# Kernel optimization log

Measured on AMD Instinct MI355X. Metric: run time of the kernel, lower is better.

## Reference

```python
import jax, jax.numpy as jnp
import numpy as np
import math

DIM = 512
HEADS = 8
DH = DIM // HEADS          # 64 = dim_head
M = 17                     # num_landmarks
PINV_ITERS = 6
RES_K = 33                 # residual depthwise conv kernel (lucidrains default)


def layer_norm(x, g, b, eps=1e-5):
    mu = x.mean(-1, keepdims=True)
    var = ((x - mu) ** 2).mean(-1, keepdims=True)
    return (x - mu) * jax.lax.rsqrt(var + eps) * g + b


def dwconv2d(x, w, b, k):
    # x: [B,C,H,W], w: [C,1,k,k] depthwise
    p = k // 2
    y = jax.lax.conv_general_dilated(x, w, (1, 1), ((p, p), (p, p)),
        dimension_numbers=('NCHW', 'OIHW', 'NCHW'), feature_group_count=x.shape[1])
    return y + b[None, :, None, None]


def moore_penrose_pinv(x, iters=PINV_ITERS):
    ax = jnp.abs(x)
    z = jnp.swapaxes(x, -1, -2) / (jnp.max(ax.sum(-1)) * jnp.max(ax.sum(-2)))
    I = jnp.eye(x.shape[-1], dtype=x.dtype)
    for _ in range(iters):
        xz = x @ z
        z = 0.25 * z @ (13 * I - xz @ (15 * I - xz @ (7 * I - xz)))
    return z


def nystrom_attn(x, qkv_w, out_w, out_b, res_w):
    # lucidrains NystromAttention, eval mode (dropout=identity), return_attn=True
    b, n, _ = x.shape
    pad = (M - n % M) % M
    xp = jnp.pad(x, ((0, 0), (pad, 0), (0, 0)))  # pad at FRONT
    q, k, v = jnp.split(xp @ qkv_w, 3, axis=-1)
    to_heads = lambda t: t.reshape(b, -1, HEADS, DH).transpose(0, 2, 1, 3)  # b h n d
    q, k, v = to_heads(q), to_heads(k), to_heads(v)
    q = q * (DH ** -0.5)
    l = (n + pad) // M
    ql = q.reshape(b, HEADS, M, l, DH).mean(3)  # landmarks b h m d
    kl = k.reshape(b, HEADS, M, l, DH).mean(3)
    a1 = jax.nn.softmax(jnp.einsum('bhid,bhjd->bhij', q, kl), axis=-1)   # [b,h,n,m]
    a2 = jax.nn.softmax(jnp.einsum('bhid,bhjd->bhij', ql, kl), axis=-1)  # [b,h,m,m]
    a3 = jax.nn.softmax(jnp.einsum('bhid,bhjd->bhij', ql, k), axis=-1)   # [b,h,m,n]
    a2i = moore_penrose_pinv(a2)
    left = a1 @ a2i                       # [b,h,n,m]
    out = left @ (a3 @ v)                 # [b,h,n,d]
    # residual depthwise conv over heads, kernel (33,1) along seq
    res = jax.lax.conv_general_dilated(v, res_w, (1, 1), ((RES_K // 2, RES_K // 2), (0, 0)),
        dimension_numbers=('NCHW', 'OIHW', 'NCHW'), feature_group_count=HEADS)
    out = out + res
    out = out.transpose(0, 2, 1, 3).reshape(b, -1, DIM)
    out = out @ out_w + out_b
    attn = left @ a3                      # [b,h,n_pad,n_pad]
    return out[:, -n:], attn


def ppeg(x, H, W, w7, b7, w5, b5, w3, b3):
    B, _, C = x.shape
    cls_t, feat = x[:, :1], x[:, 1:]
    cnn = feat.transpose(0, 2, 1).reshape(B, C, H, W)
    y = dwconv2d(cnn, w7, b7, 7) + cnn + dwconv2d(cnn, w5, b5, 5) + dwconv2d(cnn, w3, b3, 3)
    y = y.reshape(B, C, H * W).transpose(0, 2, 1)
    return jnp.concatenate([cls_t, y], axis=1)


def setup_inputs():
    key = jax.random.key(0)
    ks = jax.random.split(key, 20)
    B, N, IN, NC = 2, 2048, 1024, 2
    s = 0.02
    d = {}
    d['feats'] = jax.random.normal(ks[0], (B, N, IN), jnp.float32)
    d['fc1_w'] = jax.random.normal(ks[1], (IN, DIM), jnp.float32) * s
    d['fc1_b'] = jnp.zeros((DIM,), jnp.float32)
    d['cls_token'] = jax.random.normal(ks[2], (1, 1, DIM), jnp.float32)
    for i, pre in enumerate(['l1', 'l2']):
        o = 3 + i * 3
        d[pre + '_norm_g'] = jnp.ones((DIM,), jnp.float32)
        d[pre + '_norm_b'] = jnp.zeros((DIM,), jnp.float32)
        d[pre + '_qkv_w'] = jax.random.normal(ks[o], (DIM, 3 * DIM), jnp.float32) * s
        d[pre + '_out_w'] = jax.random.normal(ks[o + 1], (DIM, DIM), jnp.float32) * s
        d[pre + '_out_b'] = jnp.zeros((DIM,), jnp.float32)
        d[pre + '_res_w'] = jax.random.normal(ks[o + 2], (HEADS, 1, RES_K, 1), jnp.float32) * s
    for kk, kidx in zip([7, 5, 3], [9, 10, 11]):
        d['ppeg_w%d' % kk] = jax.random.normal(ks[kidx], (DIM, 1, kk, kk), jnp.float32) * s
        d['ppeg_b%d' % kk] = jnp.zeros((DIM,), jnp.float32)
    d['norm_g'] = jnp.ones((DIM,), jnp.float32)
    d['norm_b'] = jnp.zeros((DIM,), jnp.float32)
    d['fc2_w'] = jax.random.normal(ks[12], (DIM, NC), jnp.float32) * s
    d['fc2_b'] = jnp.zeros((NC,), jnp.float32)
    return d


def reference(feats, fc1_w, fc1_b, cls_token,
              l1_norm_g, l1_norm_b, l1_qkv_w, l1_out_w, l1_out_b, l1_res_w,
              l2_norm_g, l2_norm_b, l2_qkv_w, l2_out_w, l2_out_b, l2_res_w,
              ppeg_w7, ppeg_b7, ppeg_w5, ppeg_b5, ppeg_w3, ppeg_b3,
              norm_g, norm_b, fc2_w, fc2_b):
    h = jax.nn.relu(feats @ fc1_w + fc1_b)          # [B,N,512]
    N = h.shape[1]
    Hs = int(math.ceil(math.sqrt(N)))               # square grid side
    add = Hs * Hs - N
    h = jnp.concatenate([h, h[:, :add]], axis=1)    # duplicate-pad to Hs*Hs
    B = h.shape[0]
    h = jnp.concatenate([jnp.broadcast_to(cls_token, (B, 1, DIM)), h], axis=1)
    a1, aw1 = nystrom_attn(layer_norm(h, l1_norm_g, l1_norm_b), l1_qkv_w, l1_out_w, l1_out_b, l1_res_w)
    h = h + a1
    h = ppeg(h, Hs, Hs, ppeg_w7, ppeg_b7, ppeg_w5, ppeg_b5, ppeg_w3, ppeg_b3)
    a2, aw2 = nystrom_attn(layer_norm(h, l2_norm_g, l2_norm_b), l2_qkv_w, l2_out_w, l2_out_b, l2_res_w)
    h = h + a2
    h = layer_norm(h, norm_g, norm_b)[:, 0]
    logits = h @ fc2_w + fc2_b
    return logits, aw1, aw2
```

## Files before the change

### kernel.cpp

```cpp
#include <hip/hip_runtime.h>
#include <math.h>
#include <stdint.h>

#define BATCH 2
#define NIN   1024
#define NSEQ  2048
#define DIMC  512
#define NH    8
#define DHD   64
#define MLM   17
#define LBLK  125
#define SEQ   2117
#define NPAD  2125
#define PAD0  8
#define HS    46
#define NPIX  2116
#define RA    4250
#define AWSZ  ((size_t)BATCH*NH*NPAD*NPAD)

typedef _Float16 half8 __attribute__((ext_vector_type(8)));
typedef float    floatx4 __attribute__((ext_vector_type(4)));

__device__ __forceinline__ void store_hl(_Float16* __restrict__ xh, _Float16* __restrict__ xl,
                                         int c, int ra, float v)
{
    _Float16 hv = (_Float16)v;
    size_t o = ((size_t)(c >> 3) * RA + ra) * 8 + (c & 7);
    xh[o] = hv;
    xl[o] = (_Float16)(v - (float)hv);
}

__global__ void convA_kernel(const float* __restrict__ X, _Float16* __restrict__ hi,
                             _Float16* __restrict__ lo, int R, int K)
{
    int GK = K >> 3;
    size_t idx = (size_t)blockIdx.x * 256 + threadIdx.x;
    if (idx >= (size_t)R * GK) return;
    int r = (int)(idx % R); int gk = (int)(idx / R);
    const float* s = X + (size_t)r * K + gk * 8;
    half8 h, l;
    #pragma unroll
    for (int j = 0; j < 8; ++j) {
        float x = s[j];
        _Float16 hh = (_Float16)x;
        h[j] = hh;
        l[j] = (_Float16)(x - (float)hh);
    }
    *(half8*)(hi + idx * 8) = h;
    *(half8*)(lo + idx * 8) = l;
}

__global__ void convB_kernel(const float* __restrict__ X, _Float16* __restrict__ hi,
                             _Float16* __restrict__ lo, int N, int K)
{
    int GK = K >> 3;
    size_t idx = (size_t)blockIdx.x * 256 + threadIdx.x;
    if (idx >= (size_t)N * GK) return;
    int n = (int)(idx % N); int gk = (int)(idx / N);
    const float* s = X + (size_t)(gk * 8) * N + n;
    half8 h, l;
    #pragma unroll
    for (int j = 0; j < 8; ++j) {
        float x = s[(size_t)j * N];
        _Float16 hh = (_Float16)x;
        h[j] = hh;
        l[j] = (_Float16)(x - (float)hh);
    }
    *(half8*)(hi + idx * 8) = h;
    *(half8*)(lo + idx * 8) = l;
}

__global__ __launch_bounds__(256) void gemm_mfma(
    const _Float16* __restrict__ Ah, const _Float16* __restrict__ Al,
    const _Float16* __restrict__ Bh, const _Float16* __restrict__ Bl,
    const float* __restrict__ bias, float* __restrict__ C,
    int Mn, int Nn, int Kn, int relu,
    int split, float* __restrict__ qp, float* __restrict__ kp, float* __restrict__ vp)
{
    __shared__ _Float16 sA[2][2][4][128][8];
    __shared__ _Float16 sB[2][2][4][128][8];
    const int tid = threadIdx.x;
    const int wv = tid >> 6, ln = tid & 63;
    const int m0 = blockIdx.y * 128, n0 = blockIdx.x * 128;
    const int wm = (wv >> 1) * 64, wn = (wv & 1) * 64;
    const int g = ln >> 4, rr = ln & 15;

    floatx4 acc[4][4];
    #pragma unroll
    for (int m = 0; m < 4; ++m)
        #pragma unroll
        for (int n = 0; n < 4; ++n)
            acc[m][n] = (floatx4){0.f, 0.f, 0.f, 0.f};

    auto STAGE = [&](int bf, int gk0) {
        #pragma unroll
        for (int q2 = 0; q2 < 8; ++q2) {
            int c = wv + q2 * 4;
            int arr = c >> 3, gg = (c >> 1) & 3, hf = c & 1;
            const _Float16* base = (arr == 0) ? Ah : (arr == 1) ? Al : (arr == 2) ? Bh : Bl;
            int Rdim = (arr < 2) ? Mn : Nn;
            int rg = ((arr < 2) ? m0 : n0) + hf * 64 + ln;
            if (arr < 2 && rg >= Mn) rg = Mn - 1;
            const _Float16* src = base + ((size_t)(gk0 + gg) * Rdim + rg) * 8;
            _Float16* dst = (arr == 0) ? &sA[bf][0][gg][hf * 64][0] :
                            (arr == 1) ? &sA[bf][1][gg][hf * 64][0] :
                            (arr == 2) ? &sB[bf][0][gg][hf * 64][0] :
                                         &sB[bf][1][gg][hf * 64][0];
            __builtin_amdgcn_global_load_lds(
                (__attribute__((address_space(1))) void*)(uintptr_t)src,
                (__attribute__((address_space(3))) void*)dst, 16, 0, 0);
        }
    };

    const int nt = Kn >> 5;
    STAGE(0, 0);
    __syncthreads();
    for (int t = 0; t < nt; ++t) {
        const int cur = t & 1;
        if (t + 1 < nt) STAGE(cur ^ 1, (t + 1) * 4);
        half8 a_h[4], a_l[4], b_h[4], b_l[4];
        #pragma unroll
        for (int m = 0; m < 4; ++m) {
            a_h[m] = *(const half8*)&sA[cur][0][g][wm + m * 16 + rr][0];
            a_l[m] = *(const half8*)&sA[cur][1][g][wm + m * 16 + rr][0];
        }
        #pragma unroll
        for (int n = 0; n < 4; ++n) {
            b_h[n] = *(const half8*)&sB[cur][0][g][wn + n * 16 + rr][0];
            b_l[n] = *(const half8*)&sB[cur][1][g][wn + n * 16 + rr][0];
        }
        #pragma unroll
        for (int m = 0; m < 4; ++m)
            #pragma unroll
            for (int n = 0; n < 4; ++n) {
                acc[m][n] = __builtin_amdgcn_mfma_f32_16x16x32_f16(a_h[m], b_h[n], acc[m][n], 0, 0, 0);
                acc[m][n] = __builtin_amdgcn_mfma_f32_16x16x32_f16(a_l[m], b_h[n], acc[m][n], 0, 0, 0);
                acc[m][n] = __builtin_amdgcn_mfma_f32_16x16x32_f16(a_h[m], b_l[n], acc[m][n], 0, 0, 0);
            }
        __syncthreads();
    }

    const int rq = ln >> 4;
    if (!split) {
        #pragma unroll
        for (int n = 0; n < 4; ++n) {
            int col = n0 + wn + n * 16 + rr;
            float bv = bias ? bias[col] : 0.f;
            #pragma unroll
            for (int m = 0; m < 4; ++m) {
                #pragma unroll
                for (int r = 0; r < 4; ++r) {
                    int row = m0 + wm + m * 16 + rq * 4 + r;
                    if (row < Mn) {
                        float vv = acc[m][n][r] + bv;
                        if (relu) vv = fmaxf(vv, 0.f);
                        C[(size_t)row * Nn + col] = vv;
                    }
                }
            }
        }
    } else {
        #pragma unroll
        for (int n = 0; n < 4; ++n) {
            int col = n0 + wn + n * 16 + rr;
            int sect = col >> 9, hh = (col >> 6) & 7, dd = col & 63;
            float* dstb = (sect == 0) ? qp : (sect == 1) ? kp : vp;
            float sc = (sect == 0) ? 0.125f : 1.f;
            #pragma unroll
            for (int m = 0; m < 4; ++m) {
                #pragma unroll
                for (int r = 0; r < 4; ++r) {
                    int row = m0 + wm + m * 16 + rq * 4 + r;
                    if (row < Mn) {
                        int b = (row >= NPAD) ? 1 : 0;
                        int i = row - b * NPAD;
                        dstb[(((size_t)(b * NH + hh)) * NPAD + i) * DHD + dd] = acc[m][n][r] * sc;
                    }
                }
            }
        }
    }
}

__global__ void buildh_kernel(const float* __restrict__ h0, const float* __restrict__ cls,
                              float* __restrict__ h)
{
    size_t e4 = (size_t)blockIdx.x*256 + threadIdx.x;
    if (e4 >= (size_t)BATCH*SEQ*DIMC/4) return;
    int c4 = (int)(e4 % (DIMC/4)); size_t r = e4 / (DIMC/4);
    int t = (int)(r % SEQ); int b = (int)(r / SEQ);
    float4 val;
    if (t == 0) val = ((const float4*)cls)[c4];
    else {
        int n = t - 1;
        if (n >= NSEQ) n -= NSEQ;
        val = ((const float4*)h0)[((size_t)(b*NSEQ + n))*(DIMC/4) + c4];
    }
    ((float4*)h)[e4] = val;
}

__global__ void ln_pad_kernel(const float* __restrict__ h, const float* __restrict__ g,
                              const float* __restrict__ bta,
                              _Float16* __restrict__ xh, _Float16* __restrict__ xl)
{
    int r = blockIdx.x; int b = blockIdx.y; int t = threadIdx.x;
    int ra = b*NPAD + r;
    if (r < PAD0) {
        store_hl(xh, xl, t, ra, 0.f);
        store_hl(xh, xl, t + 256, ra, 0.f);
        return;
    }
    const float* x = &h[((size_t)(b*SEQ + r-PAD0))*DIMC];
    __shared__ float ws[4];
    int wid = t >> 6, ln = t & 63;
    float x0 = x[t], x1 = x[t+256];
    float s = x0 + x1;
    #pragma unroll
    for (int m = 1; m < 64; m <<= 1) s += __shfl_xor(s, m, 64);
    if (ln == 0) ws[wid] = s;
    __syncthreads();
    float mu = (ws[0]+ws[1]+ws[2]+ws[3]) * (1.f/512.f);
    float d0 = x0-mu, d1 = x1-mu;
    float vv = d0*d0 + d1*d1;
    #pragma unroll
    for (int m = 1; m < 64; m <<= 1) vv += __shfl_xor(vv, m, 64);
    __syncthreads();
    if (ln == 0) ws[wid] = vv;
    __syncthreads();
    float rstd = 1.0f / sqrtf((ws[0]+ws[1]+ws[2]+ws[3])*(1.f/512.f) + 1e-5f);
    store_hl(xh, xl, t,       ra, d0*rstd*g[t]     + bta[t]);
    store_hl(xh, xl, t + 256, ra, d1*rstd*g[t+256] + bta[t+256]);
}

__global__ void landmark_kernel(const float* __restrict__ q, const float* __restrict__ k,
                                float* __restrict__ ql, float* __restrict__ kl)
{
    int m = blockIdx.x, h = blockIdx.y, b = blockIdx.z, d = threadIdx.x;
    int bh = b*NH + h;
    size_t base = ((size_t)bh*NPAD + m*LBLK)*DHD + d;
    float sq = 0.f, sk = 0.f;
    for (int r=0;r<LBLK;++r){ sq += q[base + (size_t)r*DHD]; sk += k[base + (size_t)r*DHD]; }
    size_t o = ((size_t)bh*MLM + m)*DHD + d;
    ql[o] = sq / 125.f; kl[o] = sk / 125.f;
}

__global__ void a1_left_kernel(const float* __restrict__ q, const float* __restrict__ kl,
                               const float* __restrict__ a2i, float* __restrict__ left)
{
    int i = blockIdx.x, h = blockIdx.y, b = blockIdx.z;
    int bh = b*NH + h; int lane = threadIdx.x;
    __shared__ alignas(16) float qrow[64];
    __shared__ float dots[MLM];
    __shared__ float arow[MLM];
    qrow[lane] = q[((size_t)bh*NPAD + i)*DHD + lane];
    __syncthreads();
    if (lane < MLM) {
        const float4* kr4 = (const float4*)&kl[((size_t)bh*MLM + lane)*DHD];
        const float4* q4 = (const float4*)qrow;
        float acc = 0.f;
        #pragma unroll
        for (int d4=0; d4<16; ++d4) {
            float4 a = q4[d4], bb = kr4[d4];
            acc += a.x*bb.x + a.y*bb.y + a.z*bb.z + a.w*bb.w;
        }
        dots[lane] = acc;
    }
    __syncthreads();
    if (lane < MLM) {
        float mx = -1e30f;
        for (int u=0;u<MLM;++u) mx = fmaxf(mx, dots[u]);
        float s = 0.f;
        for (int u=0;u<MLM;++u) s += expf(dots[u]-mx);
        arow[lane] = expf(dots[lane]-mx)/s;
    }
    __syncthreads();
    if (lane < MLM) {
        const float* zi = &a2i[(size_t)bh*MLM*MLM];
        float acc = 0.f;
        for (int k2=0;k2<MLM;++k2) acc += arow[k2]*zi[k2*MLM + lane];
        left[((size_t)bh*NPAD + i)*MLM + lane] = acc;
    }
}

__global__ void a2_kernel(const float* __restrict__ ql, const float* __restrict__ kl,
                          float* __restrict__ a2)
{
    int bh = blockIdx.x; int t = threadIdx.x;
    __shared__ float s[MLM*MLM];
    if (t < MLM*MLM) {
        int m = t/MLM, j = t%MLM;
        const float* qr = &ql[((size_t)bh*MLM+m)*DHD];
        const float* kr = &kl[((size_t)bh*MLM+j)*DHD];
        float acc=0.f; for(int d=0;d<DHD;++d) acc += qr[d]*kr[d];
        s[t] = acc;
    }
    __syncthreads();
    if (t < MLM*MLM) {
        int m = t/MLM;
        float mx=-1e30f; for(int u=0;u<MLM;++u) mx=fmaxf(mx, s[m*MLM+u]);
        float sm=0.f; for(int u=0;u<MLM;++u) sm += expf(s[m*MLM+u]-mx);
        a2[(size_t)bh*MLM*MLM + t] = expf(s[t]-mx)/sm;
    }
}

__global__ void a3_kernel(const float* __restrict__ ql, const float* __restrict__ k,
                          float* __restrict__ a3)
{
    int m = blockIdx.x, h = blockIdx.y, b = blockIdx.z;
    int bh = b*NH + h; int tid = threadIdx.x;
    __shared__ alignas(16) float qlrow[64];
    __shared__ float buf[NPAD];
    __shared__ float red[256];
    if (tid < 64) qlrow[tid] = ql[((size_t)bh*MLM+m)*DHD + tid];
    __syncthreads();
    for (int j = tid; j < NPAD; j += 256) {
        const float4* kr4 = (const float4*)&k[((size_t)bh*NPAD + j)*DHD];
        const float4* q4 = (const float4*)qlrow;
        float acc = 0.f;
        #pragma unroll
        for (int d4=0; d4<16; ++d4) {
            float4 kk = kr4[d4], qq = q4[d4];
            acc += qq.x*kk.x + qq.y*kk.y + qq.z*kk.z + qq.w*kk.w;
        }
        buf[j] = acc;
    }
    __syncthreads();
    float mx = -1e30f;
    for (int j = tid; j < NPAD; j += 256) mx = fmaxf(mx, buf[j]);
    red[tid] = mx; __syncthreads();
    for (int s=128;s>0;s>>=1){ if(tid<s) red[tid]=fmaxf(red[tid],red[tid+s]); __syncthreads(); }
    mx = red[0]; __syncthreads();
    float sm = 0.f;
    for (int j = tid; j < NPAD; j += 256) sm += expf(buf[j]-mx);
    red[tid] = sm; __syncthreads();
    for (int s=128;s>0;s>>=1){ if(tid<s) red[tid]+=red[tid+s]; __syncthreads(); }
    sm = red[0];
    for (int j = tid; j < NPAD; j += 256)
        a3[((size_t)bh*MLM+m)*NPAD + j] = expf(buf[j]-mx)/sm;
}

__global__ void pinv_kernel(const float* __restrict__ a2, float* __restrict__ a2i)
{
    int bh = blockIdx.x; int t = threadIdx.x;
    __shared__ float x[289], z[289], xz[289], w1[289], w2[289];
    __shared__ float red[320], red2[320];
    float rs = -1e30f, cs = -1e30f;
    if (t < BATCH*NH*MLM) {
        int m2 = t/MLM, i2 = t%MLM;
        const float* xx = &a2[(size_t)m2*MLM*MLM];
        float r=0.f, c=0.f;
        for (int j=0;j<MLM;++j){ r += fabsf(xx[i2*MLM+j]); c += fabsf(xx[j*MLM+i2]); }
        rs = r; cs = c;
    }
    red[t] = rs; red2[t] = cs; __syncthreads();
    for (int s=256;s>0;s>>=1){
        if (t<s && t+s<320){ red[t]=fmaxf(red[t],red[t+s]); red2[t]=fmaxf(red2[t],red2[t+s]); }
        __syncthreads();
    }
    float scal = 1.f/(red[0]*red2[0]);

    int i = t/MLM, j = t%MLM;
    bool act = t < MLM*MLM;
    if (act) x[t] = a2[(size_t)bh*MLM*MLM + t];
    __syncthreads();
    if (act) z[t] = x[j*MLM+i] * scal;
    __syncthreads();
    for (int it=0; it<6; ++it) {
        if (act){ float a=0.f; for(int k2=0;k2<MLM;++k2) a += x[i*MLM+k2]*z[k2*MLM+j]; xz[t]=a; }
        __syncthreads();
        if (act){ w1[t] = (i==j?7.f:0.f) - xz[t]; }
        __syncthreads();
        if (act){ float a=0.f; for(int k2=0;k2<MLM;++k2) a += xz[i*MLM+k2]*w1[k2*MLM+j]; w2[t]=a; }
        __syncthreads();
        if (act){ w1[t] = (i==j?15.f:0.f) - w2[t]; }
        __syncthreads();
        if (act){ float a=0.f; for(int k2=0;k2<MLM;++k2) a += xz[i*MLM+k2]*w1[k2*MLM+j]; w2[t]=a; }
        __syncthreads();
        if (act){ w1[t] = (i==j?13.f:0.f) - w2[t]; }
        __syncthreads();
        if (act){ float a=0.f; for(int k2=0;k2<MLM;++k2) a += z[i*MLM+k2]*w1[k2*MLM+j]; w2[t]=0.25f*a; }
        __syncthreads();
        if (act) z[t] = w2[t];
        __syncthreads();
    }
    if (act) a2i[(size_t)bh*MLM*MLM + t] = z[t];
}

__global__ void a3v_kernel(const float* __restrict__ a3, const float* __restrict__ v,
                           float* __restrict__ a3v)
{
    int m = blockIdx.x, h = blockIdx.y, b = blockIdx.z, d = threadIdx.x;
    int bh = b*NH + h;
    const float* ar = &a3[((size_t)bh*MLM+m)*NPAD];
    const float* vb = &v[(size_t)bh*NPAD*DHD + d];
    float acc = 0.f;
    for (int j=0;j<NPAD;++j) acc += ar[j]*vb[(size_t)j*DHD];
    a3v[((size_t)bh*MLM+m)*DHD + d] = acc;
}

__global__ void headout_kernel(const float* __restrict__ left, const float* __restrict__ a3v,
                               const float* __restrict__ v, const float* __restrict__ res_w,
                               _Float16* __restrict__ hh, _Float16* __restrict__ hl)
{
    int i = blockIdx.x, h = blockIdx.y, b = blockIdx.z, t = threadIdx.x;
    int bh = b*NH + h;
    __shared__ float lrow[MLM];
    __shared__ float rw[33];
    if (t < MLM) lrow[t] = left[((size_t)bh*NPAD+i)*MLM+t];
    if (t < 33)  rw[t] = res_w[h*33 + t];
    __syncthreads();
    float acc = 0.f;
    for (int m2=0;m2<MLM;++m2) acc += lrow[m2]*a3v[((size_t)bh*MLM+m2)*DHD+t];
    for (int s=0;s<33;++s) {
        int ii = i + s - 16;
        if (ii >= 0 && ii < NPAD) acc += rw[s]*v[((size_t)bh*NPAD+ii)*DHD+t];
    }
    store_hl(hh, hl, h*DHD + t, b*NPAD + i, acc);
}

__global__ __launch_bounds__(256) void attn_out_kernel(const float* __restrict__ left,
                                                       const float* __restrict__ a3,
                                                       float* __restrict__ aw)
{
    int bh = blockIdx.z; int i0 = blockIdx.y*64; int j0 = blockIdx.x*512;
    int t = threadIdx.x;
    __shared__ float lrows[64][20];
    for (int u = t; u < 64*MLM; u += 256) {
        int ii = u / MLM, kk = u % MLM;
        int gi = i0 + ii;
        lrows[ii][kk] = (gi < NPAD) ? left[((size_t)bh*NPAD + gi)*MLM + kk] : 0.f;
    }
    __syncthreads();
    int j1 = j0 + t, j2 = j0 + 256 + t;
    float c1[MLM], c2[MLM];
    #pragma unroll
    for (int kk = 0; kk < MLM; ++kk) {
        c1[kk] = (j1 < NPAD) ? a3[((size_t)bh*MLM + kk)*NPAD + j1] : 0.f;
        c2[kk] = (j2 < NPAD) ? a3[((size_t)bh*MLM + kk)*NPAD + j2] : 0.f;
    }
    int imax = NPAD - i0; if (imax > 64) imax = 64;
    for (int ii = 0; ii < imax; ++ii) {
        float lv[17];
        *(float4*)&lv[0]  = *(const float4*)&lrows[ii][0];
        *(float4*)&lv[4]  = *(const float4*)&lrows[ii][4];
        *(float4*)&lv[8]  = *(const float4*)&lrows[ii][8];
        *(float4*)&lv[12] = *(const float4*)&lrows[ii][12];
        lv[16] = lrows[ii][16];
        float s1 = 0.f, s2 = 0.f;
        #pragma unroll
        for (int kk = 0; kk < MLM; ++kk) { s1 += lv[kk]*c1[kk]; s2 += lv[kk]*c2[kk]; }
        size_t ob = ((size_t)bh*NPAD + (i0+ii))*NPAD;
        if (j1 < NPAD) aw[ob + j1] = s1;
        if (j2 < NPAD) aw[ob + j2] = s2;
    }
}

__global__ void add_res_kernel(float* __restrict__ h, const float* __restrict__ proj)
{
    size_t e4 = (size_t)blockIdx.x*256 + threadIdx.x;
    if (e4 >= (size_t)BATCH*SEQ*DIMC/4) return;
    int c4 = (int)(e4 % (DIMC/4)); size_t r = e4 / (DIMC/4);
    int tt = (int)(r % SEQ); int b = (int)(r / SEQ);
    float4 p = ((const float4*)proj)[((size_t)(b*NPAD + PAD0 + tt))*(DIMC/4) + c4];
    float4* hp = &((float4*)h)[e4];
    float4 hv = *hp;
    hv.x += p.x; hv.y += p.y; hv.z += p.z; hv.w += p.w;
    *hp = hv;
}

__global__ void transpose_h2im(const float* __restrict__ h, float* __restrict__ im)
{
    __shared__ float tile[32][33];
    int p0 = blockIdx.x*32, c0 = blockIdx.y*32, b = blockIdx.z;
    int tx = threadIdx.x & 31, ty = threadIdx.x >> 5;
    #pragma unroll
    for (int i=0;i<32;i+=8) {
        int p = p0 + ty + i;
        if (p < NPIX) tile[ty+i][tx] = h[((size_t)(b*SEQ) + 1 + p)*DIMC + c0 + tx];
    }
    __syncthreads();
    #pragma unroll
    for (int i=0;i<32;i+=8) {
        int c = c0 + ty + i, p = p0 + tx;
        if (p < NPIX) im[((size_t)(b*DIMC) + c)*NPIX + p] = tile[tx][ty+i];
    }
}

__global__ void ppeg_conv_kernel(const float* __restrict__ im,
                                 const float* __restrict__ w7, const float* __restrict__ b7,
                                 const float* __restrict__ w5, const float* __restrict__ b5,
                                 const float* __restrict__ w3, const float* __restrict__ b3,
                                 float* __restrict__ im2)
{
    int c = blockIdx.x; int b = blockIdx.y; int t = threadIdx.x;
    __shared__ float img[NPIX];
    __shared__ float wf[49+25+9];
    const float* src = &im[((size_t)(b*DIMC+c))*NPIX];
    for (int p=t; p<NPIX; p+=256) img[p] = src[p];
    if (t < 49) wf[t] = w7[c*49+t];
    else if (t >= 64 && t < 64+25) wf[49 + (t-64)] = w5[c*25 + (t-64)];
    else if (t >= 96 && t < 96+9)  wf[74 + (t-96)] = w3[c*9 + (t-96)];
    __syncthreads();
    float bias = b7[c] + b5[c] + b3[c];
    for (int p=t; p<NPIX; p+=256) {
        int y = p/HS, x = p%HS;
        float acc = img[p] + bias;
        for (int dy=-3; dy<=3; ++dy){ int yy=y+dy; if (yy<0||yy>=HS) continue;
            for (int dx=-3; dx<=3; ++dx){ int xx=x+dx; if (xx<0||xx>=HS) continue;
                acc += wf[(dy+3)*7+(dx+3)]*img[yy*HS+xx]; } }
        for (int dy=-2; dy<=2; ++dy){ int yy=y+dy; if (yy<0||yy>=HS) continue;
            for (int dx=-2; dx<=2; ++dx){ int xx=x+dx; if (xx<0||xx>=HS) continue;
                acc += wf[49+(dy+2)*5+(dx+2)]*img[yy*HS+xx]; } }
        for (int dy=-1; dy<=1; ++dy){ int yy=y+dy; if (yy<0||yy>=HS) continue;
            for (int dx=-1; dx<=1; ++dx){ int xx=x+dx; if (xx<0||xx>=HS) continue;
                acc += wf[74+(dy+1)*3+(dx+1)]*img[yy*HS+xx]; } }
        im2[((size_t)(b*DIMC)+c)*NPIX + p] = acc;
    }
}

__global__ void transpose_im2h(const float* __restrict__ im2, float* __restrict__ h)
{
    __shared__ float tile[32][33];
    int p0 = blockIdx.x*32, c0 = blockIdx.y*32, b = blockIdx.z;
    int tx = threadIdx.x & 31, ty = threadIdx.x >> 5;
    #pragma unroll
    for (int i=0;i<32;i+=8) {
        int c = c0 + ty + i, p = p0 + tx;
        if (p < NPIX) tile[ty+i][tx] = im2[((size_t)(b*DIMC) + c)*NPIX + p];
    }
    __syncthreads();
    #pragma unroll
    for (int i=0;i<32;i+=8) {
        int p = p0 + ty + i;
        if (p < NPIX) h[((size_t)(b*SEQ) + 1 + p)*DIMC + c0 + tx] = tile[tx][ty+i];
    }
}

__global__ void final_kernel(const float* __restrict__ h, const float* __restrict__ g,
                             const float* __restrict__ bta, const float* __restrict__ fc2w,
                             const float* __restrict__ fc2b, float* __restrict__ out)
{
    int b = blockIdx.x; int t = threadIdx.x;
    __shared__ float red[512];
    const float* x = &h[(size_t)b*SEQ*DIMC];
    float xv = x[t];
    red[t] = xv; __syncthreads();
    for (int s=256;s>0;s>>=1){ if(t<s) red[t]+=red[t+s]; __syncthreads(); }
    float mu = red[0]/512.f; __syncthreads();
    float d = xv - mu;
    red[t] = d*d; __syncthreads();
    for (int s=256;s>0;s>>=1){ if(t<s) red[t]+=red[t+s]; __syncthreads(); }
    float var = red[0]/512.f; __syncthreads();
    float hn = d * (1.f/sqrtf(var+1e-5f)) * g[t] + bta[t];
    for (int c=0;c<2;++c) {
        red[t] = hn * fc2w[t*2+c]; __syncthreads();
        for (int s=256;s>0;s>>=1){ if(t<s) red[t]+=red[t+s]; __syncthreads(); }
        if (t==0) out[b*2+c] = red[0] + fc2b[c];
        __syncthreads();
    }
}

extern "C" void kernel_launch(void* const* d_in, const int* in_sizes, int n_in,
                              void* d_out, int out_size, void* d_ws, size_t ws_size,
                              hipStream_t stream)
{
    (void)in_sizes; (void)n_in; (void)out_size; (void)ws_size;
    const float* feats = (const float*)d_in[0];
    const float* fc1_w = (const float*)d_in[1];
    const float* fc1_b = (const float*)d_in[2];
    const float* cls   = (const float*)d_in[3];
    const float* ln_g[2]  = {(const float*)d_in[4],  (const float*)d_in[10]};
    const float* ln_b[2]  = {(const float*)d_in[5],  (const float*)d_in[11]};
    const float* qkv_w[2] = {(const float*)d_in[6],  (const float*)d_in[12]};
    const float* out_w[2] = {(const float*)d_in[7],  (const float*)d_in[13]};
    const float* out_b[2] = {(const float*)d_in[8],  (const float*)d_in[14]};
    const float* res_w[2] = {(const float*)d_in[9],  (const float*)d_in[15]};
    const float* w7 = (const float*)d_in[16]; const float* b7 = (const float*)d_in[17];
    const float* w5 = (const float*)d_in[18]; const float* b5 = (const float*)d_in[19];
    const float* w3 = (const float*)d_in[20]; const float* b3 = (const float*)d_in[21];
    const float* ng = (const float*)d_in[22]; const float* nb = (const float*)d_in[23];
    const float* fc2w = (const float*)d_in[24]; const float* fc2b = (const float*)d_in[25];

    float* ws = (float*)d_ws;
    size_t off = 0;
    float* h    = ws + off; off += (size_t)BATCH*SEQ*DIMC;
    float* h0   = ws + off; off += (size_t)BATCH*NSEQ*DIMC;
    float* scr  = ws + off; off += (size_t)BATCH*NPAD*1536;
    float* q    = ws + off; off += (size_t)BATCH*NH*NPAD*DHD;
    float* k    = ws + off; off += (size_t)BATCH*NH*NPAD*DHD;
    float* v    = ws + off; off += (size_t)BATCH*NH*NPAD*DHD;
    float* ql   = ws + off; off += (size_t)BATCH*NH*MLM*DHD;
    float* kl   = ws + off; off += (size_t)BATCH*NH*MLM*DHD;
    float* a2   = ws + off; off += (size_t)BATCH*NH*MLM*MLM + 15;
    float* a2i  = ws + off; off += (size_t)BATCH*NH*MLM*MLM + 15;
    float* a3   = ws + off; off += (size_t)BATCH*NH*MLM*NPAD;
    float* left = ws + off; off += (size_t)BATCH*NH*NPAD*MLM;
    float* a3v  = ws + off; off += (size_t)BATCH*NH*MLM*DHD;
    _Float16* XAh = (_Float16*)(ws + off); off += 2097152;
    _Float16* XAl = (_Float16*)(ws + off); off += 2097152;
    _Float16* WBh = (_Float16*)(ws + off); off += 393216;
    _Float16* WBl = (_Float16*)(ws + off); off += 393216;
    float* proj = scr;
    float* im   = scr + (size_t)BATCH*NPAD*DIMC;
    float* im2  = im  + (size_t)BATCH*DIMC*NPIX;

    float* outp = (float*)d_out;

    convA_kernel<<<((size_t)4096*128+255)/256, 256, 0, stream>>>(feats, XAh, XAl, 4096, NIN);
    convB_kernel<<<((size_t)512*128+255)/256, 256, 0, stream>>>(fc1_w, WBh, WBl, DIMC, NIN);
    gemm_mfma<<<dim3(DIMC/128, 4096/128), 256, 0, stream>>>(
        XAh, XAl, WBh, WBl, fc1_b, h0, BATCH*NSEQ, DIMC, NIN, 1, 0, nullptr, nullptr, nullptr);
    {
        size_t tot4 = (size_t)BATCH*SEQ*DIMC/4;
        buildh_kernel<<<(tot4+255)/256, 256, 0, stream>>>(h0, cls, h);
    }

    for (int L = 0; L < 2; ++L) {
        float* aw = outp + 4 + (size_t)L*AWSZ;
        ln_pad_kernel<<<dim3(NPAD, BATCH), 256, 0, stream>>>(h, ln_g[L], ln_b[L], XAh, XAl);
        convB_kernel<<<((size_t)1536*64+255)/256, 256, 0, stream>>>(qkv_w[L], WBh, WBl, 1536, DIMC);
        gemm_mfma<<<dim3(1536/128, (RA+127)/128), 256, 0, stream>>>(
            XAh, XAl, WBh, WBl, nullptr, nullptr, RA, 1536, DIMC, 0, 1, q, k, v);
        landmark_kernel<<<dim3(MLM, NH, BATCH), 64, 0, stream>>>(q, k, ql, kl);
        a2_kernel<<<dim3(BATCH*NH), 320, 0, stream>>>(ql, kl, a2);
        a3_kernel<<<dim3(MLM, NH, BATCH), 256, 0, stream>>>(ql, k, a3);
        pinv_kernel<<<BATCH*NH, 320, 0, stream>>>(a2, a2i);
        a1_left_kernel<<<dim3(NPAD, NH, BATCH), 64, 0, stream>>>(q, kl, a2i, left);
        a3v_kernel<<<dim3(MLM, NH, BATCH), 64, 0, stream>>>(a3, v, a3v);
        headout_kernel<<<dim3(NPAD, NH, BATCH), 64, 0, stream>>>(left, a3v, v, res_w[L], XAh, XAl);
        attn_out_kernel<<<dim3((NPAD+511)/512, (NPAD+63)/64, BATCH*NH), 256, 0, stream>>>(left, a3, aw);
        convB_kernel<<<((size_t)512*64+255)/256, 256, 0, stream>>>(out_w[L], WBh, WBl, DIMC, DIMC);
        gemm_mfma<<<dim3(DIMC/128, (RA+127)/128), 256, 0, stream>>>(
            XAh, XAl, WBh, WBl, out_b[L], proj, RA, DIMC, DIMC, 0, 0, nullptr, nullptr, nullptr);
        {
            size_t tot4 = (size_t)BATCH*SEQ*DIMC/4;
            add_res_kernel<<<(tot4+255)/256, 256, 0, stream>>>(h, proj);
        }
        if (L == 0) {
            transpose_h2im<<<dim3((NPIX+31)/32, DIMC/32, BATCH), 256, 0, stream>>>(h, im);
            ppeg_conv_kernel<<<dim3(DIMC, BATCH), 256, 0, stream>>>(im, w7, b7, w5, b5, w3, b3, im2);
            transpose_im2h<<<dim3((NPIX+31)/32, DIMC/32, BATCH), 256, 0, stream>>>(im2, h);
        }
    }
    final_kernel<<<BATCH, 512, 0, stream>>>(h, ng, nb, fc2w, fc2b, outp);
}
```

Before: 1.364 ms.

## Fuse attention small kernels, GEMM epilogues, and batch weight conversions

Converts all five weight matrices to hi/lo fp16 in one launch. The fc1 GEMM epilogue now writes straight into the padded sequence buffer (cls row plus wrap duplicates), and the out-projection GEMM epilogue adds into the residual in place, which removes the buildh and add_res kernels. a2 is folded into pinv, a3v into a3, and a1_left into headout, and landmark uses 4 waves. This cuts launches and intermediate memory traffic. In exchange some blocks do redundant work: every pinv block recomputes all 16 a2 matrices.

```diff
diff --git a/kernel.cpp b/kernel.cpp
--- a/kernel.cpp
+++ b/kernel.cpp
@@ -16,7 +16,15 @@
 #define HS    46
 #define NPIX  2116
 #define RA    4250
+#define WRAP  68
 #define AWSZ  ((size_t)BATCH*NH*NPAD*NPAD)
+
+#define WOFF_FC1  0
+#define WOFF_QKV0 524288
+#define WOFF_QKV1 1310720
+#define WOFF_OUT0 2097152
+#define WOFF_OUT1 2359296
+#define WTOT      2621440
 
 typedef _Float16 half8 __attribute__((ext_vector_type(8)));
 typedef float    floatx4 __attribute__((ext_vector_type(4)));
@@ -31,51 +39,65 @@
 }
 
 __global__ void convA_kernel(const float* __restrict__ X, _Float16* __restrict__ hi,
-                             _Float16* __restrict__ lo, int R, int K)
-{
-    int GK = K >> 3;
+                             _Float16* __restrict__ lo, const float* __restrict__ cls,
+                             float* __restrict__ h)
+{
+    const int R = 4096, K = NIN, GK = K >> 3;
+    if (blockIdx.x == 0) {
+        int b = threadIdx.x >> 7, c4 = threadIdx.x & 127;
+        ((float4*)h)[((size_t)(b * SEQ)) * (DIMC/4) + c4] = ((const float4*)cls)[c4];
+    }
     size_t idx = (size_t)blockIdx.x * 256 + threadIdx.x;
     if (idx >= (size_t)R * GK) return;
     int r = (int)(idx % R); int gk = (int)(idx / R);
     const float* s = X + (size_t)r * K + gk * 8;
-    half8 h, l;
+    half8 hv, lv;
     #pragma unroll
     for (int j = 0; j < 8; ++j) {
         float x = s[j];
         _Float16 hh = (_Float16)x;
-        h[j] = hh;
-        l[j] = (_Float16)(x - (float)hh);
-    }
-    *(half8*)(hi + idx * 8) = h;
-    *(half8*)(lo + idx * 8) = l;
-}
-
-__global__ void convB_kernel(const float* __restrict__ X, _Float16* __restrict__ hi,
-                             _Float16* __restrict__ lo, int N, int K)
-{
+        hv[j] = hh;
+        lv[j] = (_Float16)(x - (float)hh);
+    }
+    *(half8*)(hi + idx * 8) = hv;
+    *(half8*)(lo + idx * 8) = lv;
+}
+
+__global__ void convW_kernel(const float* __restrict__ s0, const float* __restrict__ s1,
+                             const float* __restrict__ s2, const float* __restrict__ s3,
+                             const float* __restrict__ s4,
+                             _Float16* __restrict__ Wh, _Float16* __restrict__ Wl)
+{
+    int job = blockIdx.y;
+    const float* S; int N, K; size_t doff;
+    if      (job == 0) { S = s0; N = 512;  K = 1024; doff = WOFF_FC1;  }
+    else if (job == 1) { S = s1; N = 1536; K = 512;  doff = WOFF_QKV0; }
+    else if (job == 2) { S = s2; N = 1536; K = 512;  doff = WOFF_QKV1; }
+    else if (job == 3) { S = s3; N = 512;  K = 512;  doff = WOFF_OUT0; }
+    else               { S = s4; N = 512;  K = 512;  doff = WOFF_OUT1; }
     int GK = K >> 3;
     size_t idx = (size_t)blockIdx.x * 256 + threadIdx.x;
     if (idx >= (size_t)N * GK) return;
     int n = (int)(idx % N); int gk = (int)(idx / N);
-    const float* s = X + (size_t)(gk * 8) * N + n;
-    half8 h, l;
+    const float* s = S + (size_t)(gk * 8) * N + n;
+    half8 hv, lv;
     #pragma unroll
     for (int j = 0; j < 8; ++j) {
         float x = s[(size_t)j * N];
         _Float16 hh = (_Float16)x;
-        h[j] = hh;
-        l[j] = (_Float16)(x - (float)hh);
-    }
-    *(half8*)(hi + idx * 8) = h;
-    *(half8*)(lo + idx * 8) = l;
+        hv[j] = hh;
+        lv[j] = (_Float16)(x - (float)hh);
+    }
+    *(half8*)(Wh + doff + idx * 8) = hv;
+    *(half8*)(Wl + doff + idx * 8) = lv;
 }
 
 __global__ __launch_bounds__(256) void gemm_mfma(
     const _Float16* __restrict__ Ah, const _Float16* __restrict__ Al,
     const _Float16* __restrict__ Bh, const _Float16* __restrict__ Bl,
     const float* __restrict__ bias, float* __restrict__ C,
-    int Mn, int Nn, int Kn, int relu,
-    int split, float* __restrict__ qp, float* __restrict__ kp, float* __restrict__ vp)
+    int Mn, int Nn, int Kn, int mode,
+    float* __restrict__ qp, float* __restrict__ kp, float* __restrict__ vp)
 {
     __shared__ _Float16 sA[2][2][4][128][8];
     __shared__ _Float16 sB[2][2][4][128][8];
@@ -141,20 +163,41 @@
     }
 
     const int rq = ln >> 4;
-    if (!split) {
+    if (mode == 2) {
         #pragma unroll
         for (int n = 0; n < 4; ++n) {
             int col = n0 + wn + n * 16 + rr;
-            float bv = bias ? bias[col] : 0.f;
+            float bv = bias[col];
+            #pragma unroll
+            for (int m = 0; m < 4; ++m) {
+                #pragma unroll
+                for (int r = 0; r < 4; ++r) {
+                    int row = m0 + wm + m * 16 + rq * 4 + r;
+                    float vv = fmaxf(acc[m][n][r] + bv, 0.f);
+                    int b = row >> 11, nn = row & 2047;
+                    C[((size_t)(b * SEQ + 1 + nn)) * DIMC + col] = vv;
+                    if (nn < WRAP)
+                        C[((size_t)(b * SEQ + 1 + NSEQ + nn)) * DIMC + col] = vv;
+                }
+            }
+        }
+    } else if (mode == 3) {
+        #pragma unroll
+        for (int n = 0; n < 4; ++n) {
+            int col = n0 + wn + n * 16 + rr;
+            float bv = bias[col];
             #pragma unroll
             for (int m = 0; m < 4; ++m) {
                 #pragma unroll
                 for (int r = 0; r < 4; ++r) {
                     int row = m0 + wm + m * 16 + rq * 4 + r;
                     if (row < Mn) {
-                        float vv = acc[m][n][r] + bv;
-                        if (relu) vv = fmaxf(vv, 0.f);
-                        C[(size_t)row * Nn + col] = vv;
+                        int b = (row >= NPAD) ? 1 : 0;
+                        int i = row - b * NPAD;
+                        if (i >= PAD0) {
+                            size_t o = ((size_t)(b * SEQ + i - PAD0)) * DIMC + col;
+                            C[o] += acc[m][n][r] + bv;
+                        }
                     }
                 }
             }
@@ -182,23 +225,6 @@
     }
 }
 
-__global__ void buildh_kernel(const float* __restrict__ h0, const float* __restrict__ cls,
-                              float* __restrict__ h)
-{
-    size_t e4 = (size_t)blockIdx.x*256 + threadIdx.x;
-    if (e4 >= (size_t)BATCH*SEQ*DIMC/4) return;
-    int c4 = (int)(e4 % (DIMC/4)); size_t r = e4 / (DIMC/4);
-    int t = (int)(r % SEQ); int b = (int)(r / SEQ);
-    float4 val;
-    if (t == 0) val = ((const float4*)cls)[c4];
-    else {
-        int n = t - 1;
-        if (n >= NSEQ) n -= NSEQ;
-        val = ((const float4*)h0)[((size_t)(b*NSEQ + n))*(DIMC/4) + c4];
-    }
-    ((float4*)h)[e4] = val;
-}
-
 __global__ void ln_pad_kernel(const float* __restrict__ h, const float* __restrict__ g,
                               const float* __restrict__ bta,
                               _Float16* __restrict__ xh, _Float16* __restrict__ xl)
@@ -235,82 +261,36 @@
 __global__ void landmark_kernel(const float* __restrict__ q, const float* __restrict__ k,
                                 float* __restrict__ ql, float* __restrict__ kl)
 {
-    int m = blockIdx.x, h = blockIdx.y, b = blockIdx.z, d = threadIdx.x;
+    int m = blockIdx.x, h = blockIdx.y, b = blockIdx.z;
+    int t = threadIdx.x;
+    int wv = t >> 6, d = t & 63;
     int bh = b*NH + h;
     size_t base = ((size_t)bh*NPAD + m*LBLK)*DHD + d;
     float sq = 0.f, sk = 0.f;
-    for (int r=0;r<LBLK;++r){ sq += q[base + (size_t)r*DHD]; sk += k[base + (size_t)r*DHD]; }
-    size_t o = ((size_t)bh*MLM + m)*DHD + d;
-    ql[o] = sq / 125.f; kl[o] = sk / 125.f;
-}
-
-__global__ void a1_left_kernel(const float* __restrict__ q, const float* __restrict__ kl,
-                               const float* __restrict__ a2i, float* __restrict__ left)
-{
-    int i = blockIdx.x, h = blockIdx.y, b = blockIdx.z;
-    int bh = b*NH + h; int lane = threadIdx.x;
-    __shared__ alignas(16) float qrow[64];
-    __shared__ float dots[MLM];
-    __shared__ float arow[MLM];
-    qrow[lane] = q[((size_t)bh*NPAD + i)*DHD + lane];
-    __syncthreads();
-    if (lane < MLM) {
-        const float4* kr4 = (const float4*)&kl[((size_t)bh*MLM + lane)*DHD];
-        const float4* q4 = (const float4*)qrow;
-        float acc = 0.f;
-        #pragma unroll
-        for (int d4=0; d4<16; ++d4) {
-            float4 a = q4[d4], bb = kr4[d4];
-            acc += a.x*bb.x + a.y*bb.y + a.z*bb.z + a.w*bb.w;
-        }
-        dots[lane] = acc;
-    }
-    __syncthreads();
-    if (lane < MLM) {
-        float mx = -1e30f;
-        for (int u=0;u<MLM;++u) mx = fmaxf(mx, dots[u]);
-        float s = 0.f;
-        for (int u=0;u<MLM;++u) s += expf(dots[u]-mx);
-        arow[lane] = expf(dots[lane]-mx)/s;
-    }
-    __syncthreads();
-    if (lane < MLM) {
-        const float* zi = &a2i[(size_t)bh*MLM*MLM];
-        float acc = 0.f;
-        for (int k2=0;k2<MLM;++k2) acc += arow[k2]*zi[k2*MLM + lane];
-        left[((size_t)bh*NPAD + i)*MLM + lane] = acc;
-    }
-}
-
-__global__ void a2_kernel(const float* __restrict__ ql, const float* __restrict__ kl,
-                          float* __restrict__ a2)
-{
-    int bh = blockIdx.x; int t = threadIdx.x;
-    __shared__ float s[MLM*MLM];
-    if (t < MLM*MLM) {
-        int m = t/MLM, j = t%MLM;
-        const float* qr = &ql[((size_t)bh*MLM+m)*DHD];
-        const float* kr = &kl[((size_t)bh*MLM+j)*DHD];
-        float acc=0.f; for(int d=0;d<DHD;++d) acc += qr[d]*kr[d];
-        s[t] = acc;
-    }
-    __syncthreads();
-    if (t < MLM*MLM) {
-        int m = t/MLM;
-        float mx=-1e30f; for(int u=0;u<MLM;++u) mx=fmaxf(mx, s[m*MLM+u]);
-        float sm=0.f; for(int u=0;u<MLM;++u) sm += expf(s[m*MLM+u]-mx);
-        a2[(size_t)bh*MLM*MLM + t] = expf(s[t]-mx)/sm;
+    for (int r = wv; r < LBLK; r += 4) {
+        sq += q[base + (size_t)r*DHD];
+        sk += k[base + (size_t)r*DHD];
+    }
+    __shared__ float rq[4][64], rk[4][64];
+    rq[wv][d] = sq; rk[wv][d] = sk;
+    __syncthreads();
+    if (wv == 0) {
+        size_t o = ((size_t)bh*MLM + m)*DHD + d;
+        ql[o] = (rq[0][d]+rq[1][d]+rq[2][d]+rq[3][d]) / 125.f;
+        kl[o] = (rk[0][d]+rk[1][d]+rk[2][d]+rk[3][d]) / 125.f;
     }
 }
 
 __global__ void a3_kernel(const float* __restrict__ ql, const float* __restrict__ k,
-                          float* __restrict__ a3)
+                          const float* __restrict__ v, float* __restrict__ a3,
+                          float* __restrict__ a3v)
 {
     int m = blockIdx.x, h = blockIdx.y, b = blockIdx.z;
     int bh = b*NH + h; int tid = threadIdx.x;
     __shared__ alignas(16) float qlrow[64];
     __shared__ float buf[NPAD];
     __shared__ float red[256];
+    __shared__ float pvred[4][64];
     if (tid < 64) qlrow[tid] = ql[((size_t)bh*MLM+m)*DHD + tid];
     __syncthreads();
     for (int j = tid; j < NPAD; j += 256) {
@@ -335,21 +315,61 @@
     red[tid] = sm; __syncthreads();
     for (int s=128;s>0;s>>=1){ if(tid<s) red[tid]+=red[tid+s]; __syncthreads(); }
     sm = red[0];
-    for (int j = tid; j < NPAD; j += 256)
-        a3[((size_t)bh*MLM+m)*NPAD + j] = expf(buf[j]-mx)/sm;
-}
-
-__global__ void pinv_kernel(const float* __restrict__ a2, float* __restrict__ a2i)
+    float inv = 1.f/sm;
+    float* a3r = &a3[((size_t)bh*MLM+m)*NPAD];
+    for (int j = tid; j < NPAD; j += 256) {
+        float pv = expf(buf[j]-mx)*inv;
+        buf[j] = pv;
+        a3r[j] = pv;
+    }
+    __syncthreads();
+    int wv = tid >> 6, ln = tid & 63;
+    int c0 = wv * 532, c1 = c0 + 532; if (c1 > NPAD) c1 = NPAD;
+    float acc = 0.f;
+    const float* vb = &v[(size_t)bh*NPAD*DHD + ln];
+    for (int j = c0; j < c1; ++j) acc += buf[j] * vb[(size_t)j*DHD];
+    pvred[wv][ln] = acc;
+    __syncthreads();
+    if (wv == 0)
+        a3v[((size_t)bh*MLM+m)*DHD + ln] = pvred[0][ln]+pvred[1][ln]+pvred[2][ln]+pvred[3][ln];
+}
+
+__global__ void pinv_kernel(const float* __restrict__ ql, const float* __restrict__ kl,
+                            float* __restrict__ a2i)
 {
     int bh = blockIdx.x; int t = threadIdx.x;
+    __shared__ float a2all[16*289];
     __shared__ float x[289], z[289], xz[289], w1[289], w2[289];
     __shared__ float red[320], red2[320];
+    for (int e = t; e < 16*289; e += 320) {
+        int g2 = e / 289, cell = e % 289, i2 = cell / MLM, j2 = cell % MLM;
+        const float4* qr = (const float4*)&ql[((size_t)g2*MLM + i2)*DHD];
+        const float4* kr = (const float4*)&kl[((size_t)g2*MLM + j2)*DHD];
+        float acc = 0.f;
+        #pragma unroll
+        for (int d4 = 0; d4 < 16; ++d4) {
+            float4 a = qr[d4], bb = kr[d4];
+            acc += a.x*bb.x + a.y*bb.y + a.z*bb.z + a.w*bb.w;
+        }
+        a2all[e] = acc;
+    }
+    __syncthreads();
+    if (t < 16*MLM) {
+        float* row = &a2all[(t/MLM)*289 + (t%MLM)*MLM];
+        float mx = row[0];
+        for (int u = 1; u < MLM; ++u) mx = fmaxf(mx, row[u]);
+        float sm = 0.f;
+        for (int u = 0; u < MLM; ++u) { float e2 = expf(row[u]-mx); row[u] = e2; sm += e2; }
+        float inv = 1.f/sm;
+        for (int u = 0; u < MLM; ++u) row[u] *= inv;
+    }
+    __syncthreads();
     float rs = -1e30f, cs = -1e30f;
-    if (t < BATCH*NH*MLM) {
-        int m2 = t/MLM, i2 = t%MLM;
-        const float* xx = &a2[(size_t)m2*MLM*MLM];
-        float r=0.f, c=0.f;
-        for (int j=0;j<MLM;++j){ r += fabsf(xx[i2*MLM+j]); c += fabsf(xx[j*MLM+i2]); }
+    if (t < 16*MLM) {
+        int g2 = t/MLM, i2 = t%MLM;
+        const float* M = &a2all[g2*289];
+        float r = 0.f, c = 0.f;
+        for (int j = 0; j < MLM; ++j) { r += fabsf(M[i2*MLM+j]); c += fabsf(M[j*MLM+i2]); }
         rs = r; cs = c;
     }
     red[t] = rs; red2[t] = cs; __syncthreads();
@@ -358,10 +378,9 @@
         __syncthreads();
     }
     float scal = 1.f/(red[0]*red2[0]);
-
     int i = t/MLM, j = t%MLM;
     bool act = t < MLM*MLM;
-    if (act) x[t] = a2[(size_t)bh*MLM*MLM + t];
+    if (act) x[t] = a2all[bh*289 + t];
     __syncthreads();
     if (act) z[t] = x[j*MLM+i] * scal;
     __syncthreads();
@@ -386,36 +405,59 @@
     if (act) a2i[(size_t)bh*MLM*MLM + t] = z[t];
 }
 
-__global__ void a3v_kernel(const float* __restrict__ a3, const float* __restrict__ v,
-                           float* __restrict__ a3v)
-{
-    int m = blockIdx.x, h = blockIdx.y, b = blockIdx.z, d = threadIdx.x;
-    int bh = b*NH + h;
-    const float* ar = &a3[((size_t)bh*MLM+m)*NPAD];
-    const float* vb = &v[(size_t)bh*NPAD*DHD + d];
-    float acc = 0.f;
-    for (int j=0;j<NPAD;++j) acc += ar[j]*vb[(size_t)j*DHD];
-    a3v[((size_t)bh*MLM+m)*DHD + d] = acc;
-}
-
-__global__ void headout_kernel(const float* __restrict__ left, const float* __restrict__ a3v,
-                               const float* __restrict__ v, const float* __restrict__ res_w,
-                               _Float16* __restrict__ hh, _Float16* __restrict__ hl)
-{
-    int i = blockIdx.x, h = blockIdx.y, b = blockIdx.z, t = threadIdx.x;
-    int bh = b*NH + h;
+__global__ void a1l_ho_kernel(const float* __restrict__ q, const float* __restrict__ kl,
+                              const float* __restrict__ a2i, const float* __restrict__ a3v,
+                              const float* __restrict__ v, const float* __restrict__ res_w,
+                              float* __restrict__ left,
+                              _Float16* __restrict__ hh, _Float16* __restrict__ hl)
+{
+    int i = blockIdx.x, h = blockIdx.y, b = blockIdx.z;
+    int bh = b*NH + h; int lane = threadIdx.x;
+    __shared__ alignas(16) float qrow[64];
+    __shared__ float dots[MLM];
+    __shared__ float arow[MLM];
     __shared__ float lrow[MLM];
     __shared__ float rw[33];
-    if (t < MLM) lrow[t] = left[((size_t)bh*NPAD+i)*MLM+t];
-    if (t < 33)  rw[t] = res_w[h*33 + t];
+    qrow[lane] = q[((size_t)bh*NPAD + i)*DHD + lane];
+    if (lane >= 17 && lane < 50) rw[lane-17] = res_w[h*33 + (lane-17)];
+    __syncthreads();
+    if (lane < MLM) {
+        const float4* kr4 = (const float4*)&kl[((size_t)bh*MLM + lane)*DHD];
+        const float4* q4 = (const float4*)qrow;
+        float acc = 0.f;
+        #pragma unroll
+        for (int d4=0; d4<16; ++d4) {
+            float4 a = q4[d4], bb = kr4[d4];
+            acc += a.x*bb.x + a.y*bb.y + a.z*bb.z + a.w*bb.w;
+        }
+        dots[lane] = acc;
+    }
+    __syncthreads();
+    if (lane < MLM) {
+        float mx = -1e30f;
+        for (int u=0;u<MLM;++u) mx = fmaxf(mx, dots[u]);
+        float s = 0.f;
+        for (int u=0;u<MLM;++u) s += expf(dots[u]-mx);
+        arow[lane] = expf(dots[lane]-mx)/s;
+    }
+    __syncthreads();
+    if (lane < MLM) {
+        const float* zi = &a2i[(size_t)bh*MLM*MLM];
+        float acc = 0.f;
+        for (int k2=0;k2<MLM;++k2) acc += arow[k2]*zi[k2*MLM + lane];
+        lrow[lane] = acc;
+        left[((size_t)bh*NPAD + i)*MLM + lane] = acc;
+    }
     __syncthreads();
     float acc = 0.f;
-    for (int m2=0;m2<MLM;++m2) acc += lrow[m2]*a3v[((size_t)bh*MLM+m2)*DHD+t];
+    const float* a3vb = &a3v[(size_t)bh*MLM*DHD];
+    #pragma unroll
+    for (int m2=0;m2<MLM;++m2) acc += lrow[m2]*a3vb[m2*DHD + lane];
     for (int s=0;s<33;++s) {
         int ii = i + s - 16;
-        if (ii >= 0 && ii < NPAD) acc += rw[s]*v[((size_t)bh*NPAD+ii)*DHD+t];
-    }
-    store_hl(hh, hl, h*DHD + t, b*NPAD + i, acc);
+        if (ii >= 0 && ii < NPAD) acc += rw[s]*v[((size_t)bh*NPAD+ii)*DHD + lane];
+    }
+    store_hl(hh, hl, h*DHD + lane, b*NPAD + i, acc);
 }
 
 __global__ __launch_bounds__(256) void attn_out_kernel(const float* __restrict__ left,
@@ -453,19 +495,6 @@
         if (j1 < NPAD) aw[ob + j1] = s1;
         if (j2 < NPAD) aw[ob + j2] = s2;
     }
-}
-
-__global__ void add_res_kernel(float* __restrict__ h, const float* __restrict__ proj)
-{
-    size_t e4 = (size_t)blockIdx.x*256 + threadIdx.x;
-    if (e4 >= (size_t)BATCH*SEQ*DIMC/4) return;
-    int c4 = (int)(e4 % (DIMC/4)); size_t r = e4 / (DIMC/4);
-    int tt = (int)(r % SEQ); int b = (int)(r / SEQ);
-    float4 p = ((const float4*)proj)[((size_t)(b*NPAD + PAD0 + tt))*(DIMC/4) + c4];
-    float4* hp = &((float4*)h)[e4];
-    float4 hv = *hp;
-    hv.x += p.x; hv.y += p.y; hv.z += p.z; hv.w += p.w;
-    *hp = hv;
 }
 
 __global__ void transpose_h2im(const float* __restrict__ h, float* __restrict__ im)
@@ -584,58 +613,47 @@
     float* ws = (float*)d_ws;
     size_t off = 0;
     float* h    = ws + off; off += (size_t)BATCH*SEQ*DIMC;
-    float* h0   = ws + off; off += (size_t)BATCH*NSEQ*DIMC;
-    float* scr  = ws + off; off += (size_t)BATCH*NPAD*1536;
+    float* im   = ws + off; off += (size_t)BATCH*DIMC*NPIX;
+    float* im2  = ws + off; off += (size_t)BATCH*DIMC*NPIX;
     float* q    = ws + off; off += (size_t)BATCH*NH*NPAD*DHD;
     float* k    = ws + off; off += (size_t)BATCH*NH*NPAD*DHD;
     float* v    = ws + off; off += (size_t)BATCH*NH*NPAD*DHD;
     float* ql   = ws + off; off += (size_t)BATCH*NH*MLM*DHD;
     float* kl   = ws + off; off += (size_t)BATCH*NH*MLM*DHD;
-    float* a2   = ws + off; off += (size_t)BATCH*NH*MLM*MLM + 15;
-    float* a2i  = ws + off; off += (size_t)BATCH*NH*MLM*MLM + 15;
+    float* a2i  = ws + off; off += (size_t)BATCH*NH*MLM*MLM + 16;
     float* a3   = ws + off; off += (size_t)BATCH*NH*MLM*NPAD;
     float* left = ws + off; off += (size_t)BATCH*NH*NPAD*MLM;
     float* a3v  = ws + off; off += (size_t)BATCH*NH*MLM*DHD;
     _Float16* XAh = (_Float16*)(ws + off); off += 2097152;
     _Float16* XAl = (_Float16*)(ws + off); off += 2097152;
-    _Float16* WBh = (_Float16*)(ws + off); off += 393216;
-    _Float16* WBl = (_Float16*)(ws + off); off += 393216;
-    float* proj = scr;
-    float* im   = scr + (size_t)BATCH*NPAD*DIMC;
-    float* im2  = im  + (size_t)BATCH*DIMC*NPIX;
+    _Float16* Wh  = (_Float16*)(ws + off); off += (WTOT+1)/2;
+    _Float16* Wl  = (_Float16*)(ws + off); off += (WTOT+1)/2;
 
     float* outp = (float*)d_out;
 
-    convA_kernel<<<((size_t)4096*128+255)/256, 256, 0, stream>>>(feats, XAh, XAl, 4096, NIN);
-    convB_kernel<<<((size_t)512*128+255)/256, 256, 0, stream>>>(fc1_w, WBh, WBl, DIMC, NIN);
+    convA_kernel<<<2048, 256, 0, stream>>>(feats, XAh, XAl, cls, h);
+    convW_kernel<<<dim3(384, 5), 256, 0, stream>>>(
+        fc1_w, qkv_w[0], qkv_w[1], out_w[0], out_w[1], Wh, Wl);
     gemm_mfma<<<dim3(DIMC/128, 4096/128), 256, 0, stream>>>(
-        XAh, XAl, WBh, WBl, fc1_b, h0, BATCH*NSEQ, DIMC, NIN, 1, 0, nullptr, nullptr, nullptr);
-    {
-        size_t tot4 = (size_t)BATCH*SEQ*DIMC/4;
-        buildh_kernel<<<(tot4+255)/256, 256, 0, stream>>>(h0, cls, h);
-    }
-
+        XAh, XAl, Wh + WOFF_FC1, Wl + WOFF_FC1, fc1_b, h, 4096, DIMC, NIN, 2,
+        nullptr, nullptr, nullptr);
+
+    const size_t qoffs[2] = {WOFF_QKV0, WOFF_QKV1};
+    const size_t ooffs[2] = {WOFF_OUT0, WOFF_OUT1};
     for (int L = 0; L < 2; ++L) {
         float* aw = outp + 4 + (size_t)L*AWSZ;
         ln_pad_kernel<<<dim3(NPAD, BATCH), 256, 0, stream>>>(h, ln_g[L], ln_b[L], XAh, XAl);
-        convB_kernel<<<((size_t)1536*64+255)/256, 256, 0, stream>>>(qkv_w[L], WBh, WBl, 1536, DIMC);
         gemm_mfma<<<dim3(1536/128, (RA+127)/128), 256, 0, stream>>>(
-            XAh, XAl, WBh, WBl, nullptr, nullptr, RA, 1536, DIMC, 0, 1, q, k, v);
-        landmark_kernel<<<dim3(MLM, NH, BATCH), 64, 0, stream>>>(q, k, ql, kl);
-        a2_kernel<<<dim3(BATCH*NH), 320, 0, stream>>>(ql, kl, a2);
-        a3_kernel<<<dim3(MLM, NH, BATCH), 256, 0, stream>>>(ql, k, a3);
-        pinv_kernel<<<BATCH*NH, 320, 0, stream>>>(a2, a2i);
-        a1_left_kernel<<<dim3(NPAD, NH, BATCH), 64, 0, stream>>>(q, kl, a2i, left);
-        a3v_kernel<<<dim3(MLM, NH, BATCH), 64, 0, stream>>>(a3, v, a3v);
-        headout_kernel<<<dim3(NPAD, NH, BATCH), 64, 0, stream>>>(left, a3v, v, res_w[L], XAh, XAl);
+            XAh, XAl, Wh + qoffs[L], Wl + qoffs[L], nullptr, nullptr, RA, 1536, DIMC, 1, q, k, v);
+        landmark_kernel<<<dim3(MLM, NH, BATCH), 256, 0, stream>>>(q, k, ql, kl);
+        pinv_kernel<<<BATCH*NH, 320, 0, stream>>>(ql, kl, a2i);
+        a3_kernel<<<dim3(MLM, NH, BATCH), 256, 0, stream>>>(ql, k, v, a3, a3v);
+        a1l_ho_kernel<<<dim3(NPAD, NH, BATCH), 64, 0, stream>>>(
+            q, kl, a2i, a3v, v, res_w[L], left, XAh, XAl);
         attn_out_kernel<<<dim3((NPAD+511)/512, (NPAD+63)/64, BATCH*NH), 256, 0, stream>>>(left, a3, aw);
-        convB_kernel<<<((size_t)512*64+255)/256, 256, 0, stream>>>(out_w[L], WBh, WBl, DIMC, DIMC);
         gemm_mfma<<<dim3(DIMC/128, (RA+127)/128), 256, 0, stream>>>(
-            XAh, XAl, WBh, WBl, out_b[L], proj, RA, DIMC, DIMC, 0, 0, nullptr, nullptr, nullptr);
-        {
-            size_t tot4 = (size_t)BATCH*SEQ*DIMC/4;
-            add_res_kernel<<<(tot4+255)/256, 256, 0, stream>>>(h, proj);
-        }
+            XAh, XAl, Wh + ooffs[L], Wl + ooffs[L], out_b[L], h, RA, DIMC, DIMC, 3,
+            nullptr, nullptr, nullptr);
         if (L == 0) {
             transpose_h2im<<<dim3((NPIX+31)/32, DIMC/32, BATCH), 256, 0, stream>>>(h, im);
             ppeg_conv_kernel<<<dim3(DIMC, BATCH), 256, 0, stream>>>(im, w7, b7, w5, b5, w3, b3, im2);
```

Result: slower. 1.627 ms (+19.3%).
